# Optimization experiments

Measured on AMD Instinct MI355X. Metric: run time of the kernel, lower is better.

## Reference

```python
import jax, jax.numpy as jnp
import numpy as np

N_NODES = 50000
N_EDGES = 600000
D = 128


def gcn_conv(x, src, dst, W, b, n_nodes):
    """PyG GCNConv: h = D^-1/2 (A+I) D^-1/2 (x @ W) + b, messages src->dst."""
    h = x @ W  # [N, out]
    # add self loops (weight 1)
    loop = jnp.arange(n_nodes, dtype=src.dtype)
    s = jnp.concatenate([src, loop])
    d = jnp.concatenate([dst, loop])
    w = jnp.ones(s.shape[0], dtype=x.dtype)
    deg = jax.ops.segment_sum(w, d, num_segments=n_nodes)  # in-degree at target
    dinv = jnp.where(deg > 0, jax.lax.rsqrt(deg), 0.0).astype(x.dtype)
    norm = dinv[s] * w * dinv[d]  # [E+N]
    msg = h[s] * norm[:, None]  # gather + scale
    out = jax.ops.segment_sum(msg, d, num_segments=n_nodes)  # scatter-add
    return out + b


def setup_inputs() -> dict:
    key = jax.random.key(0)
    k1, k2, k3, k4, k5, k6 = jax.random.split(key, 6)
    x = jax.random.normal(k1, (N_NODES, D), dtype=jnp.float32)
    edge_index = jax.random.randint(k2, (2, N_EDGES), 0, N_NODES, dtype=jnp.int64)
    s = (1.0 / np.sqrt(D))
    W1 = jax.random.normal(k3, (D, D), dtype=jnp.float32) * s
    b1 = jnp.zeros((D,), dtype=jnp.float32)
    W2 = jax.random.normal(k4, (D, D), dtype=jnp.float32) * s
    b2 = jnp.zeros((D,), dtype=jnp.float32)
    return {"x": x, "edge_index": edge_index, "W1": W1, "b1": b1, "W2": W2, "b2": b2}


def reference(x, edge_index, W1, b1, W2, b2):
    src, dst = edge_index[0], edge_index[1]
    # two GCN layers (order=2), ReLU activation; dropout is identity at eval
    o1 = jax.nn.relu(gcn_conv(x, src, dst, W1, b1, N_NODES))
    o2 = jax.nn.relu(gcn_conv(x, src, dst, W2, b2, N_NODES))
    # combine_mode='mean'
    return 0.5 * (o1 + o2)
```

## Files before the change

kernel.cpp:

```cpp
#include <hip/hip_runtime.h>
#include <hip/hip_bf16.h>

#define N_NODES 50000
#define N_EDGES 600000
#define D 128
#define CAP 64
#define ZSTRIDE 136

typedef __attribute__((ext_vector_type(8))) short bfrag;
typedef __attribute__((ext_vector_type(4))) float ffrag;

__device__ __forceinline__ short bf16bits(float f) {
    __hip_bfloat16 h = __float2bfloat16(f);
    return *reinterpret_cast<short*>(&h);
}
__device__ __forceinline__ float bfbits2float(short b) {
    unsigned u = ((unsigned)(unsigned short)b) << 16;
    return __uint_as_float(u);
}

__device__ __forceinline__ unsigned norm_cnt(unsigned raw) {
    return raw - (raw >= 0x80000000u ? 0xAAAAAAAAu : 0u);
}

__global__ __launch_bounds__(256, 8) void prep_kernel(
    const float* __restrict__ x, const int* __restrict__ ei,
    const float* __restrict__ W1, const float* __restrict__ W2,
    unsigned* __restrict__ cnt, int* __restrict__ srcs,
    __hip_bfloat162* __restrict__ xs, short* __restrict__ wpack)
{
    int idx = blockIdx.x * 256 + threadIdx.x;

    int es = 0, ed = 0;
    bool edge = idx < N_EDGES;
    if (edge) {
        es = ei[idx];
        ed = ei[N_EDGES + idx];
    }

    const float4* x4 = (const float4*)x;
    float4 a = x4[idx * 2];
    float4 b = x4[idx * 2 + 1];

    if (edge) {
        unsigned slot = norm_cnt(atomicAdd(&cnt[ed], 1u));
        if (slot < CAP) srcs[ed * CAP + slot] = es;
    }

    bfrag o;
    o[0] = bf16bits(a.x); o[1] = bf16bits(a.y);
    o[2] = bf16bits(a.z); o[3] = bf16bits(a.w);
    o[4] = bf16bits(b.x); o[5] = bf16bits(b.y);
    o[6] = bf16bits(b.z); o[7] = bf16bits(b.w);
    ((bfrag*)xs)[idx] = o;

    if (idx < 16) {
        bfrag z0;
#pragma unroll
        for (int j = 0; j < 8; ++j) z0[j] = 0;
        ((bfrag*)(xs + N_NODES * 64))[idx] = z0;
    }

    if (idx < 4096) {
        int l  = idx & 63;
        int ks = (idx >> 6) & 3;
        int c  = (idx >> 8) & 7;
        int m  = (idx >> 11) & 1;
        int n = c * 16 + (l & 15);
        int kbase = ks * 32 + (l >> 4) * 8;
        const float* W = m ? W2 : W1;
        bfrag w;
#pragma unroll
        for (int j = 0; j < 8; ++j) w[j] = bf16bits(W[(kbase + j) * D + n]);
        ((bfrag*)wpack)[idx] = w;
    }
}

__global__ __launch_bounds__(512, 2) void fused_kernel(
    const unsigned* __restrict__ cnt,
    const int* __restrict__ srcs,
    const __hip_bfloat162* __restrict__ xs,
    const short* __restrict__ wpack,
    const float* __restrict__ b1,
    const float* __restrict__ b2,
    float* __restrict__ out)
{
    __shared__ __align__(16) short zs16[32 * ZSTRIDE];
    const int base = blockIdx.x * 32;
    const int t = threadIdx.x;
    const int lane = t & 63;
    const int g = t >> 6;
    const int rg = g >> 2;
    const int gc = g & 3;
    const int p = lane & 15;
    const int q = lane >> 4;

    int sreg[4];
    unsigned degc[4];
    float dvr[4];
#pragma unroll
    for (int rr = 0; rr < 4; ++rr) {
        const int node = base + rg * 16 + gc * 4 + rr;
        unsigned deg = norm_cnt(cnt[node]);
        dvr[rr] = rsqrtf((float)(deg + 1));
        degc[rr] = deg < CAP ? deg : CAP;
        sreg[rr] = srcs[node * CAP + lane];
    }
    unsigned mx = 0;
#pragma unroll
    for (int rr = 0; rr < 4; ++rr) {
        unsigned n8 = (degc[rr] + 7u) & ~7u;
        mx = n8 > mx ? n8 : mx;
    }

    float acc[4][8];
#pragma unroll
    for (int rr = 0; rr < 4; ++rr)
#pragma unroll
        for (int j = 0; j < 8; ++j) acc[rr][j] = 0.f;

    for (unsigned e = 0; e < mx; e += 8) {
        int sA[4], sB[4];
        bool mA[4], mB[4];
#pragma unroll
        for (int rr = 0; rr < 4; ++rr) {
            int iA = __shfl(sreg[rr], (int)e + q, 64);
            int iB = __shfl(sreg[rr], (int)e + 4 + q, 64);
            mA[rr] = e + (unsigned)q < degc[rr];
            mB[rr] = e + 4u + (unsigned)q < degc[rr];
            sA[rr] = mA[rr] ? iA : N_NODES;
            sB[rr] = mB[rr] ? iB : N_NODES;
        }
        unsigned cA[4], cB[4];
#pragma unroll
        for (int rr = 0; rr < 4; ++rr) {
            cA[rr] = cnt[sA[rr]];
            cB[rr] = cnt[sB[rr]];
        }
        bfrag v0[4], v1[4];
#pragma unroll
        for (int rr = 0; rr < 4; ++rr) {
            v0[rr] = ((const bfrag*)(xs + sA[rr] * 64))[p];
            v1[rr] = ((const bfrag*)(xs + sB[rr] * 64))[p];
        }
        float wA[4], wB[4];
#pragma unroll
        for (int rr = 0; rr < 4; ++rr) {
            wA[rr] = mA[rr] ? rsqrtf((float)(norm_cnt(cA[rr]) + 1)) : 0.f;
            wB[rr] = mB[rr] ? rsqrtf((float)(norm_cnt(cB[rr]) + 1)) : 0.f;
        }
#pragma unroll
        for (int rr = 0; rr < 4; ++rr)
#pragma unroll
            for (int j = 0; j < 8; ++j)
                acc[rr][j] += wA[rr] * bfbits2float(v0[rr][j])
                            + wB[rr] * bfbits2float(v1[rr][j]);
    }

#pragma unroll
    for (int rr = 0; rr < 4; ++rr) {
        const int r = rg * 16 + gc * 4 + rr;
#pragma unroll
        for (int j = 0; j < 8; ++j) {
            acc[rr][j] += __shfl_xor(acc[rr][j], 16, 64);
            acc[rr][j] += __shfl_xor(acc[rr][j], 32, 64);
        }
        if (q == 0) {
            const int node = base + r;
            bfrag vs = ((const bfrag*)(xs + node * 64))[p];
            bfrag zo;
#pragma unroll
            for (int j = 0; j < 8; ++j)
                zo[j] = bf16bits(dvr[rr] * (acc[rr][j] + dvr[rr] * bfbits2float(vs[j])));
            *(bfrag*)&zs16[r * ZSTRIDE + p * 8] = zo;
        }
    }
    __syncthreads();

    const int m16 = lane & 15;
    const int quad = lane >> 4;
    const int c0 = 2 * gc;
    const int c1 = 2 * gc + 1;

    ffrag acc00 = {0.f, 0.f, 0.f, 0.f};
    ffrag acc01 = {0.f, 0.f, 0.f, 0.f};
    ffrag acc10 = {0.f, 0.f, 0.f, 0.f};
    ffrag acc11 = {0.f, 0.f, 0.f, 0.f};

#pragma unroll
    for (int ks = 0; ks < 4; ++ks) {
        bfrag a = *(const bfrag*)&zs16[(rg * 16 + m16) * ZSTRIDE + ks * 32 + quad * 8];

        bfrag b00 = *(const bfrag*)&wpack[((((0 * 8 + c0) * 4 + ks) * 64 + lane) * 8)];
        bfrag b01 = *(const bfrag*)&wpack[((((0 * 8 + c1) * 4 + ks) * 64 + lane) * 8)];
        bfrag b10 = *(const bfrag*)&wpack[((((1 * 8 + c0) * 4 + ks) * 64 + lane) * 8)];
        bfrag b11 = *(const bfrag*)&wpack[((((1 * 8 + c1) * 4 + ks) * 64 + lane) * 8)];

        acc00 = __builtin_amdgcn_mfma_f32_16x16x32_bf16(a, b00, acc00, 0, 0, 0);
        acc01 = __builtin_amdgcn_mfma_f32_16x16x32_bf16(a, b01, acc01, 0, 0, 0);
        acc10 = __builtin_amdgcn_mfma_f32_16x16x32_bf16(a, b10, acc10, 0, 0, 0);
        acc11 = __builtin_amdgcn_mfma_f32_16x16x32_bf16(a, b11, acc11, 0, 0, 0);
    }

    const int n0 = c0 * 16 + m16;
    const int n1 = c1 * 16 + m16;
    const float b1n0 = b1[n0], b1n1 = b1[n1];
    const float b2n0 = b2[n0], b2n1 = b2[n1];
#pragma unroll
    for (int reg = 0; reg < 4; ++reg) {
        int row = rg * 16 + quad * 4 + reg;
        int node = base + row;
        if (node < N_NODES) {
            float o0 = 0.5f * (fmaxf(acc00[reg] + b1n0, 0.f) + fmaxf(acc10[reg] + b2n0, 0.f));
            float o1 = 0.5f * (fmaxf(acc01[reg] + b1n1, 0.f) + fmaxf(acc11[reg] + b2n1, 0.f));
            out[node * D + n0] = o0;
            out[node * D + n1] = o1;
        }
    }
}

extern "C" void kernel_launch(void* const* d_in, const int* in_sizes, int n_in,
                              void* d_out, int out_size, void* d_ws, size_t ws_size,
                              hipStream_t stream) {
    const float* x  = (const float*)d_in[0];
    const int*   ei = (const int*)d_in[1];
    const float* W1 = (const float*)d_in[2];
    const float* b1 = (const float*)d_in[3];
    const float* W2 = (const float*)d_in[4];
    const float* b2 = (const float*)d_in[5];
    float* out = (float*)d_out;

    char* ws = (char*)d_ws;
    unsigned* cnt  = (unsigned*)(ws + 0);
    int*      srcs = (int*)(ws + 200704);
    __hip_bfloat162* xs = (__hip_bfloat162*)(ws + 13000704);
    short*    wpack = (short*)(ws + 25800960);

    prep_kernel<<<3125, 256, 0, stream>>>(x, ei, W1, W2, cnt, srcs, xs, wpack);
    fused_kernel<<<(N_NODES + 31) / 32, 512, 0, stream>>>(cnt, srcs, xs, wpack, b1, b2, out);
}
```

Before: 156.5 us.

## Pre-scale node features by inverse sqrt degree and store 16-bit source indices

Splits the prep kernel so edge bucketing runs first. A second pass then multiplies each node's bf16 features by its own D^-1/2 before storing them. The fused aggregation loop becomes a plain sum of gathered rows, with no per-edge degree gather or rsqrt. Source indices are stored as 16-bit values to halve the bucket footprint, which relies on the node count fitting in 16 bits. In exchange there is one extra kernel launch, the bucketing and feature conversion no longer overlap, and rounding changes slightly because the scale is applied before bf16 conversion.

Result: no change. 154.9 us (-1.0%).

```diff
diff --git a/kernel.cpp b/kernel.cpp
--- a/kernel.cpp
+++ b/kernel.cpp
@@ -23,35 +23,40 @@
     return raw - (raw >= 0x80000000u ? 0xAAAAAAAAu : 0u);
 }
 
-__global__ __launch_bounds__(256, 8) void prep_kernel(
-    const float* __restrict__ x, const int* __restrict__ ei,
+__global__ __launch_bounds__(256) void fill_kernel(
+    const int* __restrict__ ei, unsigned* __restrict__ cnt,
+    unsigned short* __restrict__ srcs)
+{
+    int e = blockIdx.x * 256 + threadIdx.x;
+    if (e < N_EDGES) {
+        int s = ei[e];
+        int d = ei[N_EDGES + e];
+        unsigned slot = norm_cnt(atomicAdd(&cnt[d], 1u));
+        if (slot < CAP) srcs[d * CAP + slot] = (unsigned short)s;
+    }
+}
+
+__global__ __launch_bounds__(256, 8) void dxw_kernel(
+    const float* __restrict__ x,
     const float* __restrict__ W1, const float* __restrict__ W2,
-    unsigned* __restrict__ cnt, int* __restrict__ srcs,
+    const unsigned* __restrict__ cnt,
     __hip_bfloat162* __restrict__ xs, short* __restrict__ wpack)
 {
     int idx = blockIdx.x * 256 + threadIdx.x;
 
-    int es = 0, ed = 0;
-    bool edge = idx < N_EDGES;
-    if (edge) {
-        es = ei[idx];
-        ed = ei[N_EDGES + idx];
-    }
+    int node = idx >> 4;
+    unsigned deg = norm_cnt(cnt[node]);
+    float dv = rsqrtf((float)(deg + 1));
 
     const float4* x4 = (const float4*)x;
     float4 a = x4[idx * 2];
     float4 b = x4[idx * 2 + 1];
 
-    if (edge) {
-        unsigned slot = norm_cnt(atomicAdd(&cnt[ed], 1u));
-        if (slot < CAP) srcs[ed * CAP + slot] = es;
-    }
-
     bfrag o;
-    o[0] = bf16bits(a.x); o[1] = bf16bits(a.y);
-    o[2] = bf16bits(a.z); o[3] = bf16bits(a.w);
-    o[4] = bf16bits(b.x); o[5] = bf16bits(b.y);
-    o[6] = bf16bits(b.z); o[7] = bf16bits(b.w);
+    o[0] = bf16bits(dv * a.x); o[1] = bf16bits(dv * a.y);
+    o[2] = bf16bits(dv * a.z); o[3] = bf16bits(dv * a.w);
+    o[4] = bf16bits(dv * b.x); o[5] = bf16bits(dv * b.y);
+    o[6] = bf16bits(dv * b.z); o[7] = bf16bits(dv * b.w);
     ((bfrag*)xs)[idx] = o;
 
     if (idx < 16) {
@@ -78,7 +83,7 @@
 
 __global__ __launch_bounds__(512, 2) void fused_kernel(
     const unsigned* __restrict__ cnt,
-    const int* __restrict__ srcs,
+    const unsigned short* __restrict__ srcs,
     const __hip_bfloat162* __restrict__ xs,
     const short* __restrict__ wpack,
     const float* __restrict__ b1,
@@ -98,13 +103,15 @@
     int sreg[4];
     unsigned degc[4];
     float dvr[4];
+    bfrag vself[4];
 #pragma unroll
     for (int rr = 0; rr < 4; ++rr) {
         const int node = base + rg * 16 + gc * 4 + rr;
         unsigned deg = norm_cnt(cnt[node]);
         dvr[rr] = rsqrtf((float)(deg + 1));
         degc[rr] = deg < CAP ? deg : CAP;
-        sreg[rr] = srcs[node * CAP + lane];
+        sreg[rr] = (int)srcs[node * CAP + lane];
+        vself[rr] = ((const bfrag*)(xs + node * 64))[p];
     }
     unsigned mx = 0;
 #pragma unroll
@@ -121,21 +128,12 @@
 
     for (unsigned e = 0; e < mx; e += 8) {
         int sA[4], sB[4];
-        bool mA[4], mB[4];
 #pragma unroll
         for (int rr = 0; rr < 4; ++rr) {
             int iA = __shfl(sreg[rr], (int)e + q, 64);
             int iB = __shfl(sreg[rr], (int)e + 4 + q, 64);
-            mA[rr] = e + (unsigned)q < degc[rr];
-            mB[rr] = e + 4u + (unsigned)q < degc[rr];
-            sA[rr] = mA[rr] ? iA : N_NODES;
-            sB[rr] = mB[rr] ? iB : N_NODES;
-        }
-        unsigned cA[4], cB[4];
-#pragma unroll
-        for (int rr = 0; rr < 4; ++rr) {
-            cA[rr] = cnt[sA[rr]];
-            cB[rr] = cnt[sB[rr]];
+            sA[rr] = (e + (unsigned)q < degc[rr]) ? iA : N_NODES;
+            sB[rr] = (e + 4u + (unsigned)q < degc[rr]) ? iB : N_NODES;
         }
         bfrag v0[4], v1[4];
 #pragma unroll
@@ -143,18 +141,11 @@
             v0[rr] = ((const bfrag*)(xs + sA[rr] * 64))[p];
             v1[rr] = ((const bfrag*)(xs + sB[rr] * 64))[p];
         }
-        float wA[4], wB[4];
-#pragma unroll
-        for (int rr = 0; rr < 4; ++rr) {
-            wA[rr] = mA[rr] ? rsqrtf((float)(norm_cnt(cA[rr]) + 1)) : 0.f;
-            wB[rr] = mB[rr] ? rsqrtf((float)(norm_cnt(cB[rr]) + 1)) : 0.f;
-        }
 #pragma unroll
         for (int rr = 0; rr < 4; ++rr)
 #pragma unroll
             for (int j = 0; j < 8; ++j)
-                acc[rr][j] += wA[rr] * bfbits2float(v0[rr][j])
-                            + wB[rr] * bfbits2float(v1[rr][j]);
+                acc[rr][j] += bfbits2float(v0[rr][j]) + bfbits2float(v1[rr][j]);
     }
 
 #pragma unroll
@@ -166,12 +157,10 @@
             acc[rr][j] += __shfl_xor(acc[rr][j], 32, 64);
         }
         if (q == 0) {
-            const int node = base + r;
-            bfrag vs = ((const bfrag*)(xs + node * 64))[p];
             bfrag zo;
 #pragma unroll
             for (int j = 0; j < 8; ++j)
-                zo[j] = bf16bits(dvr[rr] * (acc[rr][j] + dvr[rr] * bfbits2float(vs[j])));
+                zo[j] = bf16bits(dvr[rr] * (acc[rr][j] + bfbits2float(vself[rr][j])));
             *(bfrag*)&zs16[r * ZSTRIDE + p * 8] = zo;
         }
     }
@@ -231,11 +220,12 @@
     float* out = (float*)d_out;
 
     char* ws = (char*)d_ws;
-    unsigned* cnt  = (unsigned*)(ws + 0);
-    int*      srcs = (int*)(ws + 200704);
-    __hip_bfloat162* xs = (__hip_bfloat162*)(ws + 13000704);
-    short*    wpack = (short*)(ws + 25800960);
-
-    prep_kernel<<<3125, 256, 0, stream>>>(x, ei, W1, W2, cnt, srcs, xs, wpack);
+    unsigned*       cnt  = (unsigned*)(ws + 0);
+    unsigned short* srcs = (unsigned short*)(ws + 200704);
+    __hip_bfloat162* xs  = (__hip_bfloat162*)(ws + 6604800);
+    short*          wpack = (short*)(ws + 19405056);
+
+    fill_kernel<<<(N_EDGES + 255) / 256, 256, 0, stream>>>(ei, cnt, srcs);
+    dxw_kernel<<<3125, 256, 0, stream>>>(x, W1, W2, cnt, xs, wpack);
     fused_kernel<<<(N_NODES + 31) / 32, 512, 0, stream>>>(cnt, srcs, xs, wpack, b1, b2, out);
 }
```
